# Kernel optimization log

Measured on AMD Instinct MI355X. Metric: run time of the kernel, lower is better.

## Reference

```python
import jax, jax.numpy as jnp
from jax import lax
import numpy as np

B, T, H, W, CIN, F, NC = 8, 16, 32, 32, 6, 64, 10
BN_EPS = 1e-3


def _conv(x, k):
    # x: [B,H,W,Cin], k: [3,3,Cin,Cout], SAME padding
    return lax.conv_general_dilated(x, k, (1, 1), 'SAME',
                                    dimension_numbers=('NHWC', 'HWIO', 'NHWC'))


def _hard_sigmoid(x):
    return jnp.clip(0.2 * x + 0.5, 0.0, 1.0)


def _convlstm(x_seq, Wx, Wh, b):
    # x_seq: [B,T,H,W,Cin] -> [B,T,H,W,F]; keras gate order [i,f,c,o]
    nb, nt, nh, nw, _ = x_seq.shape
    nf = Wh.shape[2]
    h0 = jnp.zeros((nb, nh, nw, nf), x_seq.dtype)

    def step(carry, xt):
        h, c = carry
        z = _conv(xt, Wx) + _conv(h, Wh) + b
        i, f, g, o = jnp.split(z, 4, axis=-1)
        i, f, o = _hard_sigmoid(i), _hard_sigmoid(f), _hard_sigmoid(o)
        c = f * c + i * jnp.tanh(g)
        h = o * jnp.tanh(c)
        return (h, c), h

    _, hs = lax.scan(step, (h0, h0), jnp.moveaxis(x_seq, 1, 0))  # scan over T
    return jnp.moveaxis(hs, 0, 1)


def _bn(x, gamma, beta, mean, var):
    # inference-mode BatchNorm over channel axis, eps=1e-3 (keras default)
    inv = gamma * lax.rsqrt(var + BN_EPS)
    return (x - mean) * inv + beta


def setup_inputs() -> dict:
    key = jax.random.key(0)
    ks = jax.random.split(key, 12)
    s = 0.05
    d = {
        'inputs': jax.random.normal(ks[0], (B, T, H, W, CIN), jnp.float32),
        'l0_Wx': jax.random.normal(ks[1], (3, 3, CIN, 4 * F), jnp.float32) * s,
        'l0_Wh': jax.random.normal(ks[2], (3, 3, F, 4 * F), jnp.float32) * s,
        'l0_b': jnp.zeros((4 * F,), jnp.float32),
        'l0_gamma': jnp.ones((F,), jnp.float32),
        'l0_beta': jnp.zeros((F,), jnp.float32),
        'l0_mean': jnp.zeros((F,), jnp.float32),
        'l0_var': jnp.ones((F,), jnp.float32),
        'l1_Wx': jax.random.normal(ks[3], (3, 3, F, 4 * F), jnp.float32) * s,
        'l1_Wh': jax.random.normal(ks[4], (3, 3, F, 4 * F), jnp.float32) * s,
        'l1_b': jnp.zeros((4 * F,), jnp.float32),
        'l1_gamma': jnp.ones((F,), jnp.float32),
        'l1_beta': jnp.zeros((F,), jnp.float32),
        'l1_mean': jnp.zeros((F,), jnp.float32),
        'l1_var': jnp.ones((F,), jnp.float32),
        'dense_W': jax.random.normal(ks[5], (F, NC), jnp.float32) * s,
        'dense_b': jnp.zeros((NC,), jnp.float32),
    }
    return d


def reference(inputs, l0_Wx, l0_Wh, l0_b, l0_gamma, l0_beta, l0_mean, l0_var,
              l1_Wx, l1_Wh, l1_b, l1_gamma, l1_beta, l1_mean, l1_var,
              dense_W, dense_b):
    x = _convlstm(inputs, l0_Wx, l0_Wh, l0_b)
    x = _bn(x, l0_gamma, l0_beta, l0_mean, l0_var)
    x = _convlstm(x, l1_Wx, l1_Wh, l1_b)
    x = _bn(x, l1_gamma, l1_beta, l1_mean, l1_var)
    x = jax.nn.softmax(jnp.einsum('bthwf,fc->bthwc', x, dense_W) + dense_b, axis=-1)
    return jnp.mean(x, axis=(1, 2, 3))  # GlobalAveragePooling3D -> [B, NC]
```

## Files before the change

kernel.cpp:

```cpp
#include <hip/hip_runtime.h>
#include <math.h>

typedef __attribute__((ext_vector_type(8))) short short8v;
typedef __attribute__((ext_vector_type(4))) float float4v;

constexpr int Bsz = 8, Tn = 16, CINc = 6, Fc = 64, NCc = 10;
constexpr int PIX = 8192;
constexpr float BN_EPS = 1e-3f;

constexpr int FR_L0X = 0;
constexpr int FR_L0H = 16384;
constexpr int FR_L1X = 163840;
constexpr int FR_L1H = 311296;
constexpr int FR_TOTAL = 458752;

__device__ __forceinline__ ushort f2bf(float f) {
    union { float f; unsigned u; } v; v.f = f;
    unsigned r = v.u + 0x7FFFu + ((v.u >> 16) & 1u);
    return (ushort)(r >> 16);
}
__device__ __forceinline__ float bf2f(ushort u) {
    union { unsigned u; float f; } v; v.u = ((unsigned)u) << 16; return v.f;
}
__device__ __forceinline__ float hsig(float x) {
    return fminf(fmaxf(0.2f * x + 0.5f, 0.0f), 1.0f);
}

#define GLDS(srcp, dstp) \
    __builtin_amdgcn_global_load_lds((const __attribute__((address_space(1))) void*)(srcp), \
                                     (__attribute__((address_space(3))) void*)(dstp), 16, 0, 0)

__global__ __launch_bounds__(256) void prep_x(const float* __restrict__ in,
                                              ushort* __restrict__ xb) {
    int o = blockIdx.x * 256 + threadIdx.x;
    if (o >= Tn * PIX * CINc) return;
    int t = o / (PIX * CINc);
    int rem = o - t * (PIX * CINc);
    int pix = rem / CINc, c = rem - pix * CINc;
    int b = pix >> 10, p = pix & 1023;
    xb[o] = f2bf(in[((b * Tn + t) * 1024 + p) * CINc + c]);
}

__global__ __launch_bounds__(256) void prep_w(const float* __restrict__ W0x,
                                              const float* __restrict__ W0h,
                                              const float* __restrict__ W1x,
                                              const float* __restrict__ W1h,
                                              ushort* __restrict__ F) {
    int o = blockIdx.x * 256 + threadIdx.x;
    if (o >= FR_TOTAL) return;
    const float* W; int K; int base;
    if (o < FR_L0H)      { W = W0x; K = 54;  base = FR_L0X; }
    else if (o < FR_L1X) { W = W0h; K = 576; base = FR_L0H; }
    else if (o < FR_L1H) { W = W1x; K = 576; base = FR_L1X; }
    else                 { W = W1h; K = 576; base = FR_L1H; }
    int r = o - base;
    int e = r & 7, lane = (r >> 3) & 63, j = (r >> 9) & 7, nh = (r >> 12) & 1, kc = r >> 13;
    int nt = ((j >> 1) << 2) + nh * 2 + (j & 1);
    int k = kc * 32 + ((lane >> 4) * 4) + (e & 3) + 16 * (e >> 2);
    int n = nt * 16 + (lane & 15);
    F[o] = (k < K) ? f2bf(W[k * 256 + n]) : (ushort)0;
}

__global__ __launch_bounds__(640) void prep_dense(
    const float* __restrict__ dW, const float* __restrict__ dB,
    const float* __restrict__ g, const float* __restrict__ be,
    const float* __restrict__ mn, const float* __restrict__ vr,
    float* __restrict__ dWf, float* __restrict__ dBf)
{
    __shared__ float sc[64], sh[64];
    int tid = threadIdx.x;
    if (tid < 64) {
        float s = g[tid] * rsqrtf(vr[tid] + BN_EPS);
        sc[tid] = s; sh[tid] = be[tid] - mn[tid] * s;
    }
    __syncthreads();
    if (tid < 640) { int f = tid / 10; dWf[tid] = sc[f] * dW[tid]; }
    if (tid < NCc) {
        float a = dB[tid];
        for (int f = 0; f < 64; ++f) a += sh[f] * dW[f * 10 + tid];
        dBf[tid] = a;
    }
}

__global__ __launch_bounds__(256) void init_zero(float* c0, float* c1,
                                                 ushort* h0, ushort* h1,
                                                 ushort* h0b, ushort* h1b, float* out) {
    int i = blockIdx.x * 256 + threadIdx.x;
    if (i < PIX * Fc) { c0[i] = 0.f; c1[i] = 0.f; h0[i] = 0; h1[i] = 0; h0b[i] = 0; h1b[i] = 0; }
    if (i < Bsz * NCc) out[i] = 0.f;
}

__global__ __launch_bounds__(256, 3) void step_tri(
    int t,
    const ushort* __restrict__ Xb,
    const ushort* __restrict__ Bf0X, const ushort* __restrict__ Bf0H,
    const float* __restrict__ b0,
    float* __restrict__ C0, const ushort* __restrict__ H0prev, ushort* __restrict__ H0cur,
    ushort* __restrict__ X1s,
    const float* __restrict__ g0, const float* __restrict__ be0,
    const float* __restrict__ mn0, const float* __restrict__ v0,
    const ushort* __restrict__ Bf1X, const ushort* __restrict__ Bf1H,
    const float* __restrict__ b1, float* __restrict__ Z1,
    float* __restrict__ C1, const ushort* __restrict__ H1prev, ushort* __restrict__ H1cur,
    ushort* __restrict__ H1s)
{
    const int grp = blockIdx.x >> 8;
    int s;
    if (grp == 0)      { s = t;     if (s >= Tn) return; }
    else if (grp == 1) { s = t - 1; if (s < 0 || s >= Tn) return; }
    else               { s = t - 2; if (s < 0 || s >= Tn) return; }

    __shared__ ushort Hh[136 * 68];
    __shared__ ushort Xh[136 * 8];
    __shared__ ushort Bs[2][8192];

    const int tid = threadIdx.x;
    const int wid = tid >> 6, lane = tid & 63;
    const int wm = wid >> 1, wn = wid & 1;
    const int bid = blockIdx.x & 255;
    const int bm = bid >> 1, nh = bid & 1;
    const int m0 = bm * 64;
    const int img = m0 >> 10;
    const int py0 = (m0 & 1023) >> 5;

    const ushort* __restrict__ Xt   = Xb + s * PIX * CINc;
    const ushort* __restrict__ X1t  = X1s + (size_t)s * (PIX * Fc);
    float* __restrict__ Zp = Z1 + (((size_t)s * 128 + bm) * 2 + nh) * 8192;
    const int TOT = (grp == 0) ? 10 : 9;
    const ushort* __restrict__ Psrc = (grp == 0) ? H0prev : (grp == 1 ? X1t : H1prev);

    auto stageB = [&](int q, int buf) {
        const ushort *g0p, *g1p;
        if (grp == 0) {
            if (q == 0) { g0p = Bf0X + (nh << 12); g1p = Bf0X + ((2 + nh) << 12); }
            else { int tp = q - 1;
                   g0p = Bf0H + ((4 * tp + nh) << 12);
                   g1p = Bf0H + ((4 * tp + 2 + nh) << 12); }
        } else if (grp == 1) {
            g0p = Bf1X + ((4 * q + nh) << 12);
            g1p = Bf1X + ((4 * q + 2 + nh) << 12);
        } else {
            g0p = Bf1H + ((4 * q + nh) << 12);
            g1p = Bf1H + ((4 * q + 2 + nh) << 12);
        }
        ushort* d = &Bs[buf][0];
        GLDS(g0p + (tid << 3),         d + wid * 512);
        GLDS(g0p + ((256 + tid) << 3), d + 2048 + wid * 512);
        GLDS(g1p + (tid << 3),         d + 4096 + wid * 512);
        GLDS(g1p + ((256 + tid) << 3), d + 4096 + 2048 + wid * 512);
    };

    stageB(0, 0);
#pragma unroll
    for (int u = 0; u < 5; ++u) {
        int idx = tid + u * 256;
        if (idx < 1088) {
            int slot = idx >> 3, part = idx & 7;
            int yy = slot / 34, xx = slot - yy * 34;
            int gy = py0 - 1 + yy, gx = xx - 1;
            uint4 v = make_uint4(0u, 0u, 0u, 0u);
            if ((unsigned)gy < 32u && (unsigned)gx < 32u)
                v = *(const uint4*)(Psrc + (((img << 10) + gy * 32 + gx) << 6) + part * 8);
            ushort* d = &Hh[slot * 68 + part * 8];
            *(uint2*)(d)     = make_uint2(v.x, v.y);
            *(uint2*)(d + 4) = make_uint2(v.z, v.w);
        }
    }
    if (grp == 0) {
#pragma unroll
        for (int u = 0; u < 4; ++u) {
            int idx = tid + u * 256;
            if (idx < 816) {
                int slot = idx / 6, c = idx - slot * 6;
                int yy = slot / 34, xx = slot - yy * 34;
                int gy = py0 - 1 + yy, gx = xx - 1;
                ushort v = 0;
                if ((unsigned)gy < 32u && (unsigned)gx < 32u)
                    v = Xt[((img << 10) + gy * 32 + gx) * 6 + c];
                Xh[slot * 8 + c] = v;
            }
        }
    }

    float4v acc[8];
    if (grp == 2) {
#pragma unroll
        for (int a = 0; a < 8; ++a)
            acc[a] = *(const float4v*)(Zp + (((wid * 8 + a) * 64 + lane) << 2));
    } else {
        const float* __restrict__ bias = (grp == 0) ? b0 : b1;
        const int hch = (nh * 2 + wn) * 16 + (lane & 15);
#pragma unroll
        for (int g = 0; g < 4; ++g) {
            const float bb = bias[g * 64 + hch];
#pragma unroll
            for (int r = 0; r < 4; ++r) { acc[g * 2 + 0][r] = bb; acc[g * 2 + 1][r] = bb; }
        }
    }

    const int p0x = wm * 32 + (lane & 15);
    const int p1x = p0x + 16;
    const int y0r = p0x >> 5, x0c = p0x & 31;
    const int y1r = p1x >> 5, x1c = p1x & 31;
    const int coff = (lane >> 4) << 2;

    auto xfrag = [&](int lry, int lcx, int half) -> short8v {
        union { ushort e[8]; short8v v; } r;
#pragma unroll
        for (int e = 0; e < 8; ++e) {
            int kg = half * 32 + coff + (e & 3) + 16 * (e >> 2);
            ushort val = 0;
            if (kg < 54) {
                int tap = kg / 6, c = kg - tap * 6;
                int dy = tap / 3 - 1, dxx = tap % 3 - 1;
                val = Xh[((lry + dy + 1) * 34 + (lcx + dxx + 1)) * 8 + c];
            }
            r.e[e] = val;
        }
        return r.v;
    };

    __syncthreads();

    for (int q = 0; q < TOT; ++q) {
        if (q + 1 < TOT) stageB(q + 1, (q + 1) & 1);

        union { struct { uint2 lo, hi; } u; short8v s; } a00, a10, a01, a11;
        if (grp == 0 && q == 0) {
            a00.s = xfrag(y0r, x0c, 0); a01.s = xfrag(y0r, x0c, 1);
            a10.s = xfrag(y1r, x1c, 0); a11.s = xfrag(y1r, x1c, 1);
        } else {
            const int tap = (grp == 0) ? q - 1 : q;
            const int dy = tap / 3 - 1, dxx = tap % 3 - 1;
            const ushort* h0r = &Hh[((y0r + dy + 1) * 34 + (x0c + dxx + 1)) * 68 + coff];
            const ushort* h1r = &Hh[((y1r + dy + 1) * 34 + (x1c + dxx + 1)) * 68 + coff];
            a00.u.lo = *(const uint2*)(h0r);      a00.u.hi = *(const uint2*)(h0r + 16);
            a01.u.lo = *(const uint2*)(h0r + 32); a01.u.hi = *(const uint2*)(h0r + 48);
            a10.u.lo = *(const uint2*)(h1r);      a10.u.hi = *(const uint2*)(h1r + 16);
            a11.u.lo = *(const uint2*)(h1r + 32); a11.u.hi = *(const uint2*)(h1r + 48);
        }

        const ushort* bs = &Bs[q & 1][0];
        union { uint4 u; short8v s; } b0r[4], b1r[4];
#pragma unroll
        for (int g = 0; g < 4; ++g) {
            const int j = g * 2 + wn;
            b0r[g].u = *(const uint4*)(bs + ((j * 64 + lane) << 3));
            b1r[g].u = *(const uint4*)(bs + 4096 + ((j * 64 + lane) << 3));
        }

#pragma unroll
        for (int g = 0; g < 4; ++g) {
            acc[g * 2 + 0] = __builtin_amdgcn_mfma_f32_16x16x32_bf16(a00.s, b0r[g].s, acc[g * 2 + 0], 0, 0, 0);
            acc[g * 2 + 1] = __builtin_amdgcn_mfma_f32_16x16x32_bf16(a10.s, b0r[g].s, acc[g * 2 + 1], 0, 0, 0);
        }
#pragma unroll
        for (int g = 0; g < 4; ++g) {
            acc[g * 2 + 0] = __builtin_amdgcn_mfma_f32_16x16x32_bf16(a01.s, b1r[g].s, acc[g * 2 + 0], 0, 0, 0);
            acc[g * 2 + 1] = __builtin_amdgcn_mfma_f32_16x16x32_bf16(a11.s, b1r[g].s, acc[g * 2 + 1], 0, 0, 0);
        }

        __syncthreads();
    }

    if (grp == 1) {
#pragma unroll
        for (int a = 0; a < 8; ++a) {
            float4 o;
            o.x = acc[a][0]; o.y = acc[a][1]; o.z = acc[a][2]; o.w = acc[a][3];
            *(float4*)(Zp + (((wid * 8 + a) * 64 + lane) << 2)) = o;
        }
        return;
    }

    float* __restrict__ C  = (grp == 0) ? C0 : C1;
    ushort* __restrict__ Hc = (grp == 0) ? H0cur : H1cur;
    ushort* __restrict__ Seq = (grp == 0) ? (X1s + (size_t)s * (PIX * Fc))
                                          : (H1s + (size_t)s * (PIX * Fc));
    const int ch = (nh * 2 + wn) * 16 + (lane & 15);
    float inv = 0.f, mu = 0.f, bet = 0.f;
    if (grp == 0) {
        inv = g0[ch] * rsqrtf(v0[ch] + BN_EPS);
        mu = mn0[ch]; bet = be0[ch];
    }
#pragma unroll
    for (int mf = 0; mf < 2; ++mf) {
#pragma unroll
        for (int r = 0; r < 4; ++r) {
            const int p = m0 + wm * 32 + mf * 16 + (lane >> 4) * 4 + r;
            const int o = p * 64 + ch;
            float zi = acc[0 + mf][r];
            float zf = acc[2 + mf][r];
            float zg = acc[4 + mf][r];
            float zo = acc[6 + mf][r];
            float cv = hsig(zf) * C[o] + hsig(zi) * tanhf(zg);
            C[o] = cv;
            float h = hsig(zo) * tanhf(cv);
            Hc[o] = f2bf(h);
            Seq[o] = (grp == 0) ? f2bf((h - mu) * inv + bet) : f2bf(h);
        }
    }
}

__global__ __launch_bounds__(256) void pool_all(
    const ushort* __restrict__ H1seq, const float* __restrict__ dWf,
    const float* __restrict__ dBf, float* __restrict__ out)
{
    __shared__ float wlds[640];
    __shared__ float accs[NCc];
    const int tid = threadIdx.x;
    for (int i = tid; i < 640; i += 256) wlds[i] = dWf[i];
    if (tid < NCc) accs[tid] = 0.f;
    __syncthreads();

    const int gid = blockIdx.x * 256 + tid;
    const int b = (gid & 8191) >> 10;

    float logit[NCc];
#pragma unroll
    for (int c = 0; c < NCc; ++c) logit[c] = dBf[c];
    const ushort* hp = H1seq + (size_t)gid * Fc;
#pragma unroll
    for (int f0 = 0; f0 < 8; ++f0) {
        union { uint4 u; ushort s[8]; } hu;
        hu.u = *(const uint4*)(hp + f0 * 8);
#pragma unroll
        for (int j = 0; j < 8; ++j) {
            float v = bf2f(hu.s[j]);
            const float* w = &wlds[(f0 * 8 + j) * 10];
#pragma unroll
            for (int c = 0; c < NCc; ++c) logit[c] += v * w[c];
        }
    }
    float mx = logit[0];
#pragma unroll
    for (int c = 1; c < NCc; ++c) mx = fmaxf(mx, logit[c]);
    float p[NCc]; float ssum = 0.f;
#pragma unroll
    for (int c = 0; c < NCc; ++c) { p[c] = expf(logit[c] - mx); ssum += p[c]; }
    float invs = 1.f / ssum;

#pragma unroll
    for (int c = 0; c < NCc; ++c) {
        float v = p[c] * invs;
        v += __shfl_xor(v, 1);
        v += __shfl_xor(v, 2);
        v += __shfl_xor(v, 4);
        v += __shfl_xor(v, 8);
        v += __shfl_xor(v, 16);
        v += __shfl_xor(v, 32);
        if ((tid & 63) == 0) atomicAdd(&accs[c], v);
    }
    __syncthreads();
    if (tid < NCc)
        atomicAdd(&out[b * NCc + tid], accs[tid] * (1.0f / 16384.0f));
}

extern "C" void kernel_launch(void* const* d_in, const int* in_sizes, int n_in,
                              void* d_out, int out_size, void* d_ws, size_t ws_size,
                              hipStream_t stream) {
    const float* in    = (const float*)d_in[0];
    const float* l0Wx  = (const float*)d_in[1];
    const float* l0Wh  = (const float*)d_in[2];
    const float* l0b   = (const float*)d_in[3];
    const float* l0g   = (const float*)d_in[4];
    const float* l0be  = (const float*)d_in[5];
    const float* l0m   = (const float*)d_in[6];
    const float* l0v   = (const float*)d_in[7];
    const float* l1Wx  = (const float*)d_in[8];
    const float* l1Wh  = (const float*)d_in[9];
    const float* l1b   = (const float*)d_in[10];
    const float* l1g   = (const float*)d_in[11];
    const float* l1be  = (const float*)d_in[12];
    const float* l1m   = (const float*)d_in[13];
    const float* l1v   = (const float*)d_in[14];
    const float* dW    = (const float*)d_in[15];
    const float* dB    = (const float*)d_in[16];
    float* out = (float*)d_out;

    float* ws   = (float*)d_ws;
    float* c0   = ws;
    float* c1   = c0 + 524288;
    float* z1   = c1 + 524288;
    ushort* us  = (ushort*)(z1 + 33554432);
    ushort* h0p0 = us;
    ushort* h0p1 = h0p0 + 524288;
    ushort* h1p0 = h0p1 + 524288;
    ushort* h1p1 = h1p0 + 524288;
    ushort* xb  = h1p1 + 524288;
    ushort* x1  = xb + 786432;
    ushort* h1s = x1 + 8388608;
    ushort* wf  = h1s + 8388608;
    float* dWf  = (float*)(wf + 458752);
    float* dBf  = dWf + 640;

    ushort* h0p[2] = { h0p0, h0p1 };
    ushort* h1p[2] = { h1p0, h1p1 };

    prep_x<<<3072, 256, 0, stream>>>(in, xb);
    prep_w<<<1792, 256, 0, stream>>>(l0Wx, l0Wh, l1Wx, l1Wh, wf);
    prep_dense<<<1, 640, 0, stream>>>(dW, dB, l1g, l1be, l1m, l1v, dWf, dBf);
    init_zero<<<2048, 256, 0, stream>>>(c0, c1, h0p0, h1p0, h0p1, h1p1, out);

    for (int t = 0; t < Tn + 2; ++t) {
        step_tri<<<768, 256, 0, stream>>>(
            t, xb,
            wf + FR_L0X, wf + FR_L0H, l0b,
            c0, h0p[t & 1], h0p[(t + 1) & 1], x1,
            l0g, l0be, l0m, l0v,
            wf + FR_L1X, wf + FR_L1H, l1b, z1,
            c1, h1p[t & 1], h1p[(t + 1) & 1], h1s);
    }
    pool_all<<<512, 256, 0, stream>>>(h1s, dWf, dBf, out);
}
```

Baseline: 330.7 us.

## Load weight fragments directly into registers instead of staging through LDS

Drops the double-buffered LDS staging of weight tiles, which used global_load_lds. Each wave now loads its own B fragments straight from global memory into registers, prefetching the next tap one iteration ahead. This removes 32KB of shared memory and the per-iteration __syncthreads. In exchange it raises register pressure and issues redundant global loads, since wm pairs of waves fetch the same fragments.

```diff
diff --git a/kernel.cpp b/kernel.cpp
--- a/kernel.cpp
+++ b/kernel.cpp
@@ -25,10 +25,6 @@
 __device__ __forceinline__ float hsig(float x) {
     return fminf(fmaxf(0.2f * x + 0.5f, 0.0f), 1.0f);
 }
-
-#define GLDS(srcp, dstp) \
-    __builtin_amdgcn_global_load_lds((const __attribute__((address_space(1))) void*)(srcp), \
-                                     (__attribute__((address_space(3))) void*)(dstp), 16, 0, 0)
 
 __global__ __launch_bounds__(256) void prep_x(const float* __restrict__ in,
                                               ushort* __restrict__ xb) {
@@ -112,7 +108,6 @@
 
     __shared__ ushort Hh[136 * 68];
     __shared__ ushort Xh[136 * 8];
-    __shared__ ushort Bs[2][8192];
 
     const int tid = threadIdx.x;
     const int wid = tid >> 6, lane = tid & 63;
@@ -129,28 +124,18 @@
     const int TOT = (grp == 0) ? 10 : 9;
     const ushort* __restrict__ Psrc = (grp == 0) ? H0prev : (grp == 1 ? X1t : H1prev);
 
-    auto stageB = [&](int q, int buf) {
-        const ushort *g0p, *g1p;
+    auto bsub = [&](int q, int sub) -> const ushort* {
         if (grp == 0) {
-            if (q == 0) { g0p = Bf0X + (nh << 12); g1p = Bf0X + ((2 + nh) << 12); }
-            else { int tp = q - 1;
-                   g0p = Bf0H + ((4 * tp + nh) << 12);
-                   g1p = Bf0H + ((4 * tp + 2 + nh) << 12); }
+            if (q == 0) return Bf0X + ((sub * 2 + nh) << 12);
+            int tp = q - 1;
+            return Bf0H + ((4 * tp + sub * 2 + nh) << 12);
         } else if (grp == 1) {
-            g0p = Bf1X + ((4 * q + nh) << 12);
-            g1p = Bf1X + ((4 * q + 2 + nh) << 12);
+            return Bf1X + ((4 * q + sub * 2 + nh) << 12);
         } else {
-            g0p = Bf1H + ((4 * q + nh) << 12);
-            g1p = Bf1H + ((4 * q + 2 + nh) << 12);
-        }
-        ushort* d = &Bs[buf][0];
-        GLDS(g0p + (tid << 3),         d + wid * 512);
-        GLDS(g0p + ((256 + tid) << 3), d + 2048 + wid * 512);
-        GLDS(g1p + (tid << 3),         d + 4096 + wid * 512);
-        GLDS(g1p + ((256 + tid) << 3), d + 4096 + 2048 + wid * 512);
+            return Bf1H + ((4 * q + sub * 2 + nh) << 12);
+        }
     };
 
-    stageB(0, 0);
 #pragma unroll
     for (int u = 0; u < 5; ++u) {
         int idx = tid + u * 256;
@@ -203,6 +188,7 @@
     const int y0r = p0x >> 5, x0c = p0x & 31;
     const int y1r = p1x >> 5, x1c = p1x & 31;
     const int coff = (lane >> 4) << 2;
+    const int boff = lane << 3;
 
     auto xfrag = [&](int lry, int lcx, int half) -> short8v {
         union { ushort e[8]; short8v v; } r;
@@ -220,10 +206,31 @@
         return r.v;
     };
 
+    uint4 bc0[4], bc1[4], bn0[4], bn1[4];
+    {
+        const ushort* p0 = bsub(0, 0);
+        const ushort* p1 = bsub(0, 1);
+#pragma unroll
+        for (int g = 0; g < 4; ++g) {
+            const int jo = ((g * 2 + wn) * 64) << 3;
+            bc0[g] = *(const uint4*)(p0 + (jo >> 0) + boff);
+            bc1[g] = *(const uint4*)(p1 + (jo >> 0) + boff);
+        }
+    }
+
     __syncthreads();
 
     for (int q = 0; q < TOT; ++q) {
-        if (q + 1 < TOT) stageB(q + 1, (q + 1) & 1);
+        if (q + 1 < TOT) {
+            const ushort* p0 = bsub(q + 1, 0);
+            const ushort* p1 = bsub(q + 1, 1);
+#pragma unroll
+            for (int g = 0; g < 4; ++g) {
+                const int jo = ((g * 2 + wn) * 64) << 3;
+                bn0[g] = *(const uint4*)(p0 + jo + boff);
+                bn1[g] = *(const uint4*)(p1 + jo + boff);
+            }
+        }
 
         union { struct { uint2 lo, hi; } u; short8v s; } a00, a10, a01, a11;
         if (grp == 0 && q == 0) {
@@ -240,27 +247,22 @@
             a11.u.lo = *(const uint2*)(h1r + 32); a11.u.hi = *(const uint2*)(h1r + 48);
         }
 
-        const ushort* bs = &Bs[q & 1][0];
-        union { uint4 u; short8v s; } b0r[4], b1r[4];
+        union { uint4 u; short8v s; } bb;
 #pragma unroll
         for (int g = 0; g < 4; ++g) {
-            const int j = g * 2 + wn;
-            b0r[g].u = *(const uint4*)(bs + ((j * 64 + lane) << 3));
-            b1r[g].u = *(const uint4*)(bs + 4096 + ((j * 64 + lane) << 3));
-        }
-
+            bb.u = bc0[g];
+            acc[g * 2 + 0] = __builtin_amdgcn_mfma_f32_16x16x32_bf16(a00.s, bb.s, acc[g * 2 + 0], 0, 0, 0);
+            acc[g * 2 + 1] = __builtin_amdgcn_mfma_f32_16x16x32_bf16(a10.s, bb.s, acc[g * 2 + 1], 0, 0, 0);
+        }
 #pragma unroll
         for (int g = 0; g < 4; ++g) {
-            acc[g * 2 + 0] = __builtin_amdgcn_mfma_f32_16x16x32_bf16(a00.s, b0r[g].s, acc[g * 2 + 0], 0, 0, 0);
-            acc[g * 2 + 1] = __builtin_amdgcn_mfma_f32_16x16x32_bf16(a10.s, b0r[g].s, acc[g * 2 + 1], 0, 0, 0);
-        }
-#pragma unroll
-        for (int g = 0; g < 4; ++g) {
-            acc[g * 2 + 0] = __builtin_amdgcn_mfma_f32_16x16x32_bf16(a01.s, b1r[g].s, acc[g * 2 + 0], 0, 0, 0);
-            acc[g * 2 + 1] = __builtin_amdgcn_mfma_f32_16x16x32_bf16(a11.s, b1r[g].s, acc[g * 2 + 1], 0, 0, 0);
-        }
-
-        __syncthreads();
+            bb.u = bc1[g];
+            acc[g * 2 + 0] = __builtin_amdgcn_mfma_f32_16x16x32_bf16(a01.s, bb.s, acc[g * 2 + 0], 0, 0, 0);
+            acc[g * 2 + 1] = __builtin_amdgcn_mfma_f32_16x16x32_bf16(a11.s, bb.s, acc[g * 2 + 1], 0, 0, 0);
+        }
+
+#pragma unroll
+        for (int g = 0; g < 4; ++g) { bc0[g] = bn0[g]; bc1[g] = bn1[g]; }
     }
 
     if (grp == 1) {
```

After: 335.8 us. About the same (+1.5%).

## Retile ConvLSTM step blocks to 128 pixels by 64 gate columns; fuse prep kernels

Applied to the files above, without the earlier changes.

Each step block now covers four image rows (128 pixels) with a 16-channel slice of every gate, instead of two rows with half of the gate columns. Each wave owns one row and reads a smaller per-stage B fragment. The goal is to cut redundant halo loads of the hidden and input state per output pixel and to halve the B staging buffer in LDS. The four setup kernels (input cast, weight fragment packing, dense/BN folding, zero init) are merged into one block-partitioned launch to save launch overhead. The larger halo tile raises the cost of the prologue load in each block.

```diff
diff --git a/kernel.cpp b/kernel.cpp
--- a/kernel.cpp
+++ b/kernel.cpp
@@ -30,64 +30,65 @@
     __builtin_amdgcn_global_load_lds((const __attribute__((address_space(1))) void*)(srcp), \
                                      (__attribute__((address_space(3))) void*)(dstp), 16, 0, 0)
 
-__global__ __launch_bounds__(256) void prep_x(const float* __restrict__ in,
-                                              ushort* __restrict__ xb) {
-    int o = blockIdx.x * 256 + threadIdx.x;
-    if (o >= Tn * PIX * CINc) return;
-    int t = o / (PIX * CINc);
-    int rem = o - t * (PIX * CINc);
-    int pix = rem / CINc, c = rem - pix * CINc;
-    int b = pix >> 10, p = pix & 1023;
-    xb[o] = f2bf(in[((b * Tn + t) * 1024 + p) * CINc + c]);
-}
-
-__global__ __launch_bounds__(256) void prep_w(const float* __restrict__ W0x,
-                                              const float* __restrict__ W0h,
-                                              const float* __restrict__ W1x,
-                                              const float* __restrict__ W1h,
-                                              ushort* __restrict__ F) {
-    int o = blockIdx.x * 256 + threadIdx.x;
-    if (o >= FR_TOTAL) return;
-    const float* W; int K; int base;
-    if (o < FR_L0H)      { W = W0x; K = 54;  base = FR_L0X; }
-    else if (o < FR_L1X) { W = W0h; K = 576; base = FR_L0H; }
-    else if (o < FR_L1H) { W = W1x; K = 576; base = FR_L1X; }
-    else                 { W = W1h; K = 576; base = FR_L1H; }
-    int r = o - base;
-    int e = r & 7, lane = (r >> 3) & 63, j = (r >> 9) & 7, nh = (r >> 12) & 1, kc = r >> 13;
-    int nt = ((j >> 1) << 2) + nh * 2 + (j & 1);
-    int k = kc * 32 + ((lane >> 4) * 4) + (e & 3) + 16 * (e >> 2);
-    int n = nt * 16 + (lane & 15);
-    F[o] = (k < K) ? f2bf(W[k * 256 + n]) : (ushort)0;
-}
-
-__global__ __launch_bounds__(640) void prep_dense(
+__global__ __launch_bounds__(256) void prep_all(
+    const float* __restrict__ in, ushort* __restrict__ xb,
+    const float* __restrict__ W0x, const float* __restrict__ W0h,
+    const float* __restrict__ W1x, const float* __restrict__ W1h,
+    ushort* __restrict__ F,
     const float* __restrict__ dW, const float* __restrict__ dB,
-    const float* __restrict__ g, const float* __restrict__ be,
-    const float* __restrict__ mn, const float* __restrict__ vr,
-    float* __restrict__ dWf, float* __restrict__ dBf)
+    const float* __restrict__ g1, const float* __restrict__ be1,
+    const float* __restrict__ mn1, const float* __restrict__ vr1,
+    float* __restrict__ dWf, float* __restrict__ dBf,
+    float* __restrict__ c0, float* __restrict__ c1,
+    ushort* __restrict__ h00, ushort* __restrict__ h01,
+    ushort* __restrict__ h10, ushort* __restrict__ h11,
+    float* __restrict__ out)
 {
+    const int b = blockIdx.x, tid = threadIdx.x;
     __shared__ float sc[64], sh[64];
-    int tid = threadIdx.x;
-    if (tid < 64) {
-        float s = g[tid] * rsqrtf(vr[tid] + BN_EPS);
-        sc[tid] = s; sh[tid] = be[tid] - mn[tid] * s;
-    }
-    __syncthreads();
-    if (tid < 640) { int f = tid / 10; dWf[tid] = sc[f] * dW[tid]; }
-    if (tid < NCc) {
-        float a = dB[tid];
-        for (int f = 0; f < 64; ++f) a += sh[f] * dW[f * 10 + tid];
-        dBf[tid] = a;
-    }
-}
-
-__global__ __launch_bounds__(256) void init_zero(float* c0, float* c1,
-                                                 ushort* h0, ushort* h1,
-                                                 ushort* h0b, ushort* h1b, float* out) {
-    int i = blockIdx.x * 256 + threadIdx.x;
-    if (i < PIX * Fc) { c0[i] = 0.f; c1[i] = 0.f; h0[i] = 0; h1[i] = 0; h0b[i] = 0; h1b[i] = 0; }
-    if (i < Bsz * NCc) out[i] = 0.f;
+
+    if (b < 3072) {
+        int o = b * 256 + tid;
+        if (o < Tn * PIX * CINc) {
+            int t = o / (PIX * CINc);
+            int rem = o - t * (PIX * CINc);
+            int pix = rem / CINc, c = rem - pix * CINc;
+            int bb = pix >> 10, p = pix & 1023;
+            xb[o] = f2bf(in[((bb * Tn + t) * 1024 + p) * CINc + c]);
+        }
+    } else if (b < 4864) {
+        int o = (b - 3072) * 256 + tid;
+        if (o < FR_TOTAL) {
+            const float* W; int K; int base;
+            if (o < FR_L0H)      { W = W0x; K = 54;  base = FR_L0X; }
+            else if (o < FR_L1X) { W = W0h; K = 576; base = FR_L0H; }
+            else if (o < FR_L1H) { W = W1x; K = 576; base = FR_L1X; }
+            else                 { W = W1h; K = 576; base = FR_L1H; }
+            int r = o - base;
+            int e = r & 7, lane = (r >> 3) & 63, j = (r >> 9) & 7, nh = (r >> 12) & 1, kc = r >> 13;
+            int nt = ((j >> 1) << 2) + nh * 2 + (j & 1);
+            int k = kc * 32 + ((lane >> 4) * 4) + (e & 3) + 16 * (e >> 2);
+            int n = nt * 16 + (lane & 15);
+            F[o] = (k < K) ? f2bf(W[k * 256 + n]) : (ushort)0;
+        }
+    } else if (b < 6912) {
+        int i = (b - 4864) * 256 + tid;
+        c0[i] = 0.f; c1[i] = 0.f;
+        h00[i] = 0; h01[i] = 0; h10[i] = 0; h11[i] = 0;
+        if (b == 4864 && tid < Bsz * NCc) out[tid] = 0.f;
+    } else {
+        if (tid < 64) {
+            float s = g1[tid] * rsqrtf(vr1[tid] + BN_EPS);
+            sc[tid] = s; sh[tid] = be1[tid] - mn1[tid] * s;
+        }
+        __syncthreads();
+        for (int i = tid; i < 640; i += 256) dWf[i] = sc[i / 10] * dW[i];
+        if (tid < NCc) {
+            float a = dB[tid];
+            for (int f = 0; f < 64; ++f) a += sh[f] * dW[f * 10 + tid];
+            dBf[tid] = a;
+        }
+    }
 }
 
 __global__ __launch_bounds__(256, 3) void step_tri(
@@ -108,53 +109,52 @@
     int s;
     if (grp == 0)      { s = t;     if (s >= Tn) return; }
     else if (grp == 1) { s = t - 1; if (s < 0 || s >= Tn) return; }
-    else               { s = t - 2; if (s < 0 || s >= Tn) return; }
-
-    __shared__ ushort Hh[136 * 68];
-    __shared__ ushort Xh[136 * 8];
-    __shared__ ushort Bs[2][8192];
+    else               { s = t - 2; if (s < 0) return; }
+
+    __shared__ ushort Hh[204 * 68];
+    __shared__ ushort Xh[204 * 8];
+    __shared__ ushort Bs[2][4096];
 
     const int tid = threadIdx.x;
     const int wid = tid >> 6, lane = tid & 63;
-    const int wm = wid >> 1, wn = wid & 1;
     const int bid = blockIdx.x & 255;
-    const int bm = bid >> 1, nh = bid & 1;
-    const int m0 = bm * 64;
+    const int bm = bid >> 2, nq = bid & 3;
+    const int m0 = bm * 128;
     const int img = m0 >> 10;
     const int py0 = (m0 & 1023) >> 5;
 
     const ushort* __restrict__ Xt   = Xb + s * PIX * CINc;
     const ushort* __restrict__ X1t  = X1s + (size_t)s * (PIX * Fc);
-    float* __restrict__ Zp = Z1 + (((size_t)s * 128 + bm) * 2 + nh) * 8192;
+    float* __restrict__ Zp = Z1 + (((size_t)s * 64 + bm) * 4 + nq) * 8192;
     const int TOT = (grp == 0) ? 10 : 9;
     const ushort* __restrict__ Psrc = (grp == 0) ? H0prev : (grp == 1 ? X1t : H1prev);
 
+    const int jsel = nq & 1, nhq = nq >> 1;
+
+    auto bblock = [&](int q, int sub) -> const ushort* {
+        if (grp == 0) {
+            if (q == 0) return Bf0X + ((sub * 2 + nhq) << 12);
+            int tp = q - 1;
+            return Bf0H + ((4 * tp + 2 * sub + nhq) << 12);
+        } else if (grp == 1) {
+            return Bf1X + ((4 * q + 2 * sub + nhq) << 12);
+        }
+        return Bf1H + ((4 * q + 2 * sub + nhq) << 12);
+    };
     auto stageB = [&](int q, int buf) {
-        const ushort *g0p, *g1p;
-        if (grp == 0) {
-            if (q == 0) { g0p = Bf0X + (nh << 12); g1p = Bf0X + ((2 + nh) << 12); }
-            else { int tp = q - 1;
-                   g0p = Bf0H + ((4 * tp + nh) << 12);
-                   g1p = Bf0H + ((4 * tp + 2 + nh) << 12); }
-        } else if (grp == 1) {
-            g0p = Bf1X + ((4 * q + nh) << 12);
-            g1p = Bf1X + ((4 * q + 2 + nh) << 12);
-        } else {
-            g0p = Bf1H + ((4 * q + nh) << 12);
-            g1p = Bf1H + ((4 * q + 2 + nh) << 12);
-        }
-        ushort* d = &Bs[buf][0];
-        GLDS(g0p + (tid << 3),         d + wid * 512);
-        GLDS(g0p + ((256 + tid) << 3), d + 2048 + wid * 512);
-        GLDS(g1p + (tid << 3),         d + 4096 + wid * 512);
-        GLDS(g1p + ((256 + tid) << 3), d + 4096 + 2048 + wid * 512);
+        const int j = (wid << 1) + jsel;
+#pragma unroll
+        for (int sub = 0; sub < 2; ++sub) {
+            const ushort* src = bblock(q, sub) + (j << 9) + (lane << 3);
+            GLDS(src, &Bs[buf][(sub << 11) + (wid << 9)]);
+        }
     };
 
     stageB(0, 0);
 #pragma unroll
-    for (int u = 0; u < 5; ++u) {
+    for (int u = 0; u < 7; ++u) {
         int idx = tid + u * 256;
-        if (idx < 1088) {
+        if (idx < 1632) {
             int slot = idx >> 3, part = idx & 7;
             int yy = slot / 34, xx = slot - yy * 34;
             int gy = py0 - 1 + yy, gx = xx - 1;
@@ -168,9 +168,9 @@
     }
     if (grp == 0) {
 #pragma unroll
-        for (int u = 0; u < 4; ++u) {
+        for (int u = 0; u < 5; ++u) {
             int idx = tid + u * 256;
-            if (idx < 816) {
+            if (idx < 1224) {
                 int slot = idx / 6, c = idx - slot * 6;
                 int yy = slot / 34, xx = slot - yy * 34;
                 int gy = py0 - 1 + yy, gx = xx - 1;
@@ -182,6 +182,7 @@
         }
     }
 
+    const int ch = (nq << 4) + (lane & 15);
     float4v acc[8];
     if (grp == 2) {
 #pragma unroll
@@ -189,22 +190,18 @@
             acc[a] = *(const float4v*)(Zp + (((wid * 8 + a) * 64 + lane) << 2));
     } else {
         const float* __restrict__ bias = (grp == 0) ? b0 : b1;
-        const int hch = (nh * 2 + wn) * 16 + (lane & 15);
 #pragma unroll
         for (int g = 0; g < 4; ++g) {
-            const float bb = bias[g * 64 + hch];
+            const float bb = bias[(g << 6) + ch];
 #pragma unroll
             for (int r = 0; r < 4; ++r) { acc[g * 2 + 0][r] = bb; acc[g * 2 + 1][r] = bb; }
         }
     }
 
-    const int p0x = wm * 32 + (lane & 15);
-    const int p1x = p0x + 16;
-    const int y0r = p0x >> 5, x0c = p0x & 31;
-    const int y1r = p1x >> 5, x1c = p1x & 31;
+    const int x0 = lane & 15, x1 = x0 + 16;
     const int coff = (lane >> 4) << 2;
 
-    auto xfrag = [&](int lry, int lcx, int half) -> short8v {
+    auto xfrag = [&](int x, int half) -> short8v {
         union { ushort e[8]; short8v v; } r;
 #pragma unroll
         for (int e = 0; e < 8; ++e) {
@@ -213,7 +210,7 @@
             if (kg < 54) {
                 int tap = kg / 6, c = kg - tap * 6;
                 int dy = tap / 3 - 1, dxx = tap % 3 - 1;
-                val = Xh[((lry + dy + 1) * 34 + (lcx + dxx + 1)) * 8 + c];
+                val = Xh[((wid + dy + 1) * 34 + (x + dxx + 1)) * 8 + c];
             }
             r.e[e] = val;
         }
@@ -227,13 +224,13 @@
 
         union { struct { uint2 lo, hi; } u; short8v s; } a00, a10, a01, a11;
         if (grp == 0 && q == 0) {
-            a00.s = xfrag(y0r, x0c, 0); a01.s = xfrag(y0r, x0c, 1);
-            a10.s = xfrag(y1r, x1c, 0); a11.s = xfrag(y1r, x1c, 1);
+            a00.s = xfrag(x0, 0); a01.s = xfrag(x0, 1);
+            a10.s = xfrag(x1, 0); a11.s = xfrag(x1, 1);
         } else {
             const int tap = (grp == 0) ? q - 1 : q;
             const int dy = tap / 3 - 1, dxx = tap % 3 - 1;
-            const ushort* h0r = &Hh[((y0r + dy + 1) * 34 + (x0c + dxx + 1)) * 68 + coff];
-            const ushort* h1r = &Hh[((y1r + dy + 1) * 34 + (x1c + dxx + 1)) * 68 + coff];
+            const ushort* h0r = &Hh[((wid + dy + 1) * 34 + (x0 + dxx + 1)) * 68 + coff];
+            const ushort* h1r = &Hh[((wid + dy + 1) * 34 + (x1 + dxx + 1)) * 68 + coff];
             a00.u.lo = *(const uint2*)(h0r);      a00.u.hi = *(const uint2*)(h0r + 16);
             a01.u.lo = *(const uint2*)(h0r + 32); a01.u.hi = *(const uint2*)(h0r + 48);
             a10.u.lo = *(const uint2*)(h1r);      a10.u.hi = *(const uint2*)(h1r + 16);
@@ -244,9 +241,8 @@
         union { uint4 u; short8v s; } b0r[4], b1r[4];
 #pragma unroll
         for (int g = 0; g < 4; ++g) {
-            const int j = g * 2 + wn;
-            b0r[g].u = *(const uint4*)(bs + ((j * 64 + lane) << 3));
-            b1r[g].u = *(const uint4*)(bs + 4096 + ((j * 64 + lane) << 3));
+            b0r[g].u = *(const uint4*)(bs + (g << 9) + (lane << 3));
+            b1r[g].u = *(const uint4*)(bs + 2048 + (g << 9) + (lane << 3));
         }
 
 #pragma unroll
@@ -277,7 +273,6 @@
     ushort* __restrict__ Hc = (grp == 0) ? H0cur : H1cur;
     ushort* __restrict__ Seq = (grp == 0) ? (X1s + (size_t)s * (PIX * Fc))
                                           : (H1s + (size_t)s * (PIX * Fc));
-    const int ch = (nh * 2 + wn) * 16 + (lane & 15);
     float inv = 0.f, mu = 0.f, bet = 0.f;
     if (grp == 0) {
         inv = g0[ch] * rsqrtf(v0[ch] + BN_EPS);
@@ -287,7 +282,7 @@
     for (int mf = 0; mf < 2; ++mf) {
 #pragma unroll
         for (int r = 0; r < 4; ++r) {
-            const int p = m0 + wm * 32 + mf * 16 + (lane >> 4) * 4 + r;
+            const int p = m0 + wid * 32 + mf * 16 + (lane >> 4) * 4 + r;
             const int o = p * 64 + ch;
             float zi = acc[0 + mf][r];
             float zf = acc[2 + mf][r];
@@ -397,10 +392,9 @@
     ushort* h0p[2] = { h0p0, h0p1 };
     ushort* h1p[2] = { h1p0, h1p1 };
 
-    prep_x<<<3072, 256, 0, stream>>>(in, xb);
-    prep_w<<<1792, 256, 0, stream>>>(l0Wx, l0Wh, l1Wx, l1Wh, wf);
-    prep_dense<<<1, 640, 0, stream>>>(dW, dB, l1g, l1be, l1m, l1v, dWf, dBf);
-    init_zero<<<2048, 256, 0, stream>>>(c0, c1, h0p0, h1p0, h0p1, h1p1, out);
+    prep_all<<<6913, 256, 0, stream>>>(in, xb, l0Wx, l0Wh, l1Wx, l1Wh, wf,
+                                       dW, dB, l1g, l1be, l1m, l1v, dWf, dBf,
+                                       c0, c1, h0p0, h0p1, h1p0, h1p1, out);
 
     for (int t = 0; t < Tn + 2; ++t) {
         step_tri<<<768, 256, 0, stream>>>(
```

After: 360.9 us. 9.1% more time.
